# Kernel tuning notes

Hardware: AMD Instinct MI355X
Metric: run time of the kernel (lower is better)

## Reference

```python
import jax, jax.numpy as jnp
import numpy as np

NUM_CITIES = 88
NUM_YEARS = 6
STDDEVE = 0.01
STDDEVG = 0.1
STDDEVW = 0.1
N_ROWS = 200000


def setup_inputs() -> dict:
    key = jax.random.key(0)
    k = jax.random.split(key, 6)
    G = jax.random.normal(k[0], (N_ROWS, NUM_CITIES), dtype=jnp.float32)
    out = jax.random.normal(k[1], (N_ROWS, NUM_YEARS), dtype=jnp.float32)
    U = jax.random.normal(k[2], (N_ROWS, NUM_YEARS), dtype=jnp.float32)
    V = jax.random.normal(k[3], (N_ROWS, NUM_YEARS), dtype=jnp.float32)
    D = jax.random.normal(k[4], (N_ROWS, NUM_CITIES), dtype=jnp.float32)
    w = jax.random.normal(k[5], (N_ROWS, NUM_CITIES), dtype=jnp.float32)
    return {"G": G, "out": out, "U": U, "V": V, "D": D, "w": w}


def reference(G, out, U, V, D, w):
    # sum over first num_years-1 columns of ||U[:,i]-out[:,i]||_2^2 == Frobenius sq norm
    diff = U[:, : NUM_YEARS - 1] - out[:, : NUM_YEARS - 1]
    loss = jnp.sum(diff * diff)
    # sum_i log(||G[:,i]||_1), all 88 column L1 norms in one fused reduction
    lgg = jnp.sum(jnp.log(jnp.sum(jnp.abs(G), axis=0)))
    loss = loss + (STDDEVE ** 2) * lgg
    # ||G - w*D||_F^2 * stddevg^2 / stddeve^2
    r = G - w * D
    loss = loss + jnp.sum(r * r) * (STDDEVG ** 2 / STDDEVE ** 2)
    # ||w^2||_1 * stddeve^2 / stddevw^2
    loss = loss + jnp.sum(w * w) * (STDDEVE ** 2 / STDDEVW ** 2)
    # penalty: sum over negative entries of G, scaled by 100
    loss = loss + jnp.sum(jnp.where(G < 0, G, 0.0) * 100.0)
    return loss
```

## Files before the change

kernel.cpp:

```cpp
#include <hip/hip_runtime.h>
#include <math.h>

#define NUM_CITIES 88
#define NUM_YEARS 6
#define N_ROWS 200000

#define COL4 (NUM_CITIES / 4)
#define TOT4 (N_ROWS * COL4)
#define DIFF2 (N_ROWS * NUM_YEARS / 2)

#define NBLK 1936
#define NTHREADS (NBLK * 256)
#define NPART 92

#define TAIL_CUT (TOT4 - 8 * NTHREADS)

#define WS2_OFF (NBLK * NPART)

__global__ __launch_bounds__(256) void loss_main(
    const float* __restrict__ G,
    const float* __restrict__ outm,
    const float* __restrict__ U,
    const float* __restrict__ D,
    const float* __restrict__ w,
    float* __restrict__ ws)
{
    __shared__ float scol[NUM_CITIES];
    __shared__ float ssum[4];

    const int tid = threadIdx.x;
    const int gtid = blockIdx.x * blockDim.x + tid;
    const int c0 = (gtid % COL4) * 4;

    const float4* __restrict__ G4 = (const float4*)G;
    const float4* __restrict__ D4 = (const float4*)D;
    const float4* __restrict__ W4 = (const float4*)w;

    float4 g0 = G4[gtid + 0 * NTHREADS], g1 = G4[gtid + 1 * NTHREADS];
    float4 g2 = G4[gtid + 2 * NTHREADS], g3 = G4[gtid + 3 * NTHREADS];
    float4 g4 = G4[gtid + 4 * NTHREADS], g5 = G4[gtid + 5 * NTHREADS];
    float4 g6 = G4[gtid + 6 * NTHREADS], g7 = G4[gtid + 7 * NTHREADS];
    float4 d0 = D4[gtid + 0 * NTHREADS], d1 = D4[gtid + 1 * NTHREADS];
    float4 d2 = D4[gtid + 2 * NTHREADS], d3 = D4[gtid + 3 * NTHREADS];
    float4 d4 = D4[gtid + 4 * NTHREADS], d5 = D4[gtid + 5 * NTHREADS];
    float4 d6 = D4[gtid + 6 * NTHREADS], d7 = D4[gtid + 7 * NTHREADS];
    float4 v0 = W4[gtid + 0 * NTHREADS], v1 = W4[gtid + 1 * NTHREADS];
    float4 v2 = W4[gtid + 2 * NTHREADS], v3 = W4[gtid + 3 * NTHREADS];
    float4 v4 = W4[gtid + 4 * NTHREADS], v5 = W4[gtid + 5 * NTHREADS];
    float4 v6 = W4[gtid + 6 * NTHREADS], v7 = W4[gtid + 7 * NTHREADS];

    float ca0 = 0.f, ca1 = 0.f, ca2 = 0.f, ca3 = 0.f;
    float s_r2 = 0.f, s_w2 = 0.f, s_neg = 0.f;

#define ACC(g, d, v)                                                          \
    {                                                                         \
        ca0 += fabsf(g.x); ca1 += fabsf(g.y);                                 \
        ca2 += fabsf(g.z); ca3 += fabsf(g.w);                                 \
        float r0 = g.x - v.x * d.x, r1 = g.y - v.y * d.y;                     \
        float r2 = g.z - v.z * d.z, r3 = g.w - v.w * d.w;                     \
        s_r2 += r0 * r0 + r1 * r1 + r2 * r2 + r3 * r3;                        \
        s_w2 += v.x * v.x + v.y * v.y + v.z * v.z + v.w * v.w;                \
        s_neg += fminf(g.x, 0.f) + fminf(g.y, 0.f)                            \
               + fminf(g.z, 0.f) + fminf(g.w, 0.f);                           \
    }

    ACC(g0, d0, v0) ACC(g1, d1, v1) ACC(g2, d2, v2) ACC(g3, d3, v3)
    ACC(g4, d4, v4) ACC(g5, d5, v5) ACC(g6, d6, v6) ACC(g7, d7, v7)

    if (gtid < TAIL_CUT) {
        float4 g = G4[gtid + 8 * NTHREADS];
        float4 d = D4[gtid + 8 * NTHREADS];
        float4 v = W4[gtid + 8 * NTHREADS];
        ACC(g, d, v)
    }
#undef ACC

    const float2* __restrict__ U2 = (const float2*)U;
    const float2* __restrict__ O2 = (const float2*)outm;
    float s_diff = 0.f;
    {
        float2 u = U2[gtid], o = O2[gtid];
        float dx = u.x - o.x, dy = u.y - o.y;
        s_diff += dx * dx + ((gtid % 3 != 2) ? dy * dy : 0.f);
        const int i2 = gtid + NTHREADS;
        if (i2 < DIFF2) {
            float2 u2 = U2[i2], o2 = O2[i2];
            float ex = u2.x - o2.x, ey = u2.y - o2.y;
            s_diff += ex * ex + ((i2 % 3 != 2) ? ey * ey : 0.f);
        }
    }

    if (tid < NUM_CITIES) scol[tid] = 0.f;
    if (tid < 4) ssum[tid] = 0.f;
    __syncthreads();

    atomicAdd(&scol[c0 + 0], ca0);
    atomicAdd(&scol[c0 + 1], ca1);
    atomicAdd(&scol[c0 + 2], ca2);
    atomicAdd(&scol[c0 + 3], ca3);

    for (int off = 32; off > 0; off >>= 1) {
        s_diff += __shfl_down(s_diff, off);
        s_r2   += __shfl_down(s_r2, off);
        s_w2   += __shfl_down(s_w2, off);
        s_neg  += __shfl_down(s_neg, off);
    }
    if ((tid & 63) == 0) {
        atomicAdd(&ssum[0], s_diff);
        atomicAdd(&ssum[1], s_r2);
        atomicAdd(&ssum[2], s_w2);
        atomicAdd(&ssum[3], s_neg);
    }
    __syncthreads();

    float* dst = ws + (size_t)blockIdx.x * NPART;
    if (tid < NUM_CITIES) dst[tid] = scol[tid];
    else if (tid < NPART)  dst[tid] = ssum[tid - NUM_CITIES];
}

__global__ __launch_bounds__(256) void loss_reduce(float* __restrict__ ws)
{
    const int k = blockIdx.x;
    const int t = threadIdx.x;
    float acc = 0.f;
    for (int b = t; b < NBLK; b += 256)
        acc += ws[(size_t)b * NPART + k];
    for (int off = 32; off > 0; off >>= 1) acc += __shfl_down(acc, off);
    __shared__ float s[4];
    if ((t & 63) == 0) s[t >> 6] = acc;
    __syncthreads();
    if (t == 0) ws[WS2_OFF + k] = s[0] + s[1] + s[2] + s[3];
}

__global__ __launch_bounds__(128) void loss_finalize(
    const float* __restrict__ ws, float* __restrict__ out)
{
    __shared__ float sh[2];
    const int t = threadIdx.x;
    const float* ws2 = ws + WS2_OFF;

    float v = 0.f;
    if (t < NUM_CITIES)      v = 1e-4f * logf(ws2[t]);
    else if (t == 88)        v = ws2[88];
    else if (t == 89)        v = 100.f * ws2[89];
    else if (t == 90)        v = 0.01f * ws2[90];
    else if (t == 91)        v = 100.f * ws2[91];

    for (int off = 32; off > 0; off >>= 1) v += __shfl_down(v, off);
    if (t == 0)  sh[0] = v;
    if (t == 64) sh[1] = v;
    __syncthreads();
    if (t == 0) out[0] = sh[0] + sh[1];
}

extern "C" void kernel_launch(void* const* d_in, const int* in_sizes, int n_in,
                              void* d_out, int out_size, void* d_ws, size_t ws_size,
                              hipStream_t stream) {
    const float* G    = (const float*)d_in[0];
    const float* outm = (const float*)d_in[1];
    const float* U    = (const float*)d_in[2];
    const float* D    = (const float*)d_in[4];
    const float* w    = (const float*)d_in[5];
    float* out = (float*)d_out;
    float* ws  = (float*)d_ws;

    loss_main<<<NBLK, 256, 0, stream>>>(G, outm, U, D, w, ws);
    loss_reduce<<<NPART, 256, 0, stream>>>(ws);
    loss_finalize<<<1, 128, 0, stream>>>(ws, out);
}
```

Before: 224.8 us.

## Split G/D/w and U-out reductions into separate block groups with fewer items per thread

Restructures the main kernel so that most blocks each handle 4 float4 rows of G/D/w per thread, and a separate set of blocks handles the U-out difference with float4 loads in a grid-stride loop. The aim is to raise the number of threads and outstanding loads, and to stop the large G/D/w loads from being serialized with the small difference loads in the same thread. In exchange there are many more blocks, each doing a full shared-memory column reduction and writing 92 partials, so the second reduction pass reads about 2.4 times as many partials.

```diff
diff --git a/kernel.cpp b/kernel.cpp
--- a/kernel.cpp
+++ b/kernel.cpp
@@ -5,17 +5,17 @@
 #define NUM_YEARS 6
 #define N_ROWS 200000
 
-#define COL4 (NUM_CITIES / 4)
-#define TOT4 (N_ROWS * COL4)
-#define DIFF2 (N_ROWS * NUM_YEARS / 2)
+#define TOT4 (N_ROWS * 22)
+#define NT   (TOT4 / 4)
+#define GBLK 4297
 
-#define NBLK 1936
-#define NTHREADS (NBLK * 256)
+#define NQ4  (N_ROWS * NUM_YEARS / 4)
+#define DTHREADS 75008
+#define DBLK 293
+
+#define NBLK_TOT (GBLK + DBLK)
 #define NPART 92
-
-#define TAIL_CUT (TOT4 - 8 * NTHREADS)
-
-#define WS2_OFF (NBLK * NPART)
+#define WS2_OFF (NBLK_TOT * NPART)
 
 __global__ __launch_bounds__(256) void loss_main(
     const float* __restrict__ G,
@@ -29,75 +29,66 @@
     __shared__ float ssum[4];
 
     const int tid = threadIdx.x;
-    const int gtid = blockIdx.x * blockDim.x + tid;
-    const int c0 = (gtid % COL4) * 4;
-
-    const float4* __restrict__ G4 = (const float4*)G;
-    const float4* __restrict__ D4 = (const float4*)D;
-    const float4* __restrict__ W4 = (const float4*)w;
-
-    float4 g0 = G4[gtid + 0 * NTHREADS], g1 = G4[gtid + 1 * NTHREADS];
-    float4 g2 = G4[gtid + 2 * NTHREADS], g3 = G4[gtid + 3 * NTHREADS];
-    float4 g4 = G4[gtid + 4 * NTHREADS], g5 = G4[gtid + 5 * NTHREADS];
-    float4 g6 = G4[gtid + 6 * NTHREADS], g7 = G4[gtid + 7 * NTHREADS];
-    float4 d0 = D4[gtid + 0 * NTHREADS], d1 = D4[gtid + 1 * NTHREADS];
-    float4 d2 = D4[gtid + 2 * NTHREADS], d3 = D4[gtid + 3 * NTHREADS];
-    float4 d4 = D4[gtid + 4 * NTHREADS], d5 = D4[gtid + 5 * NTHREADS];
-    float4 d6 = D4[gtid + 6 * NTHREADS], d7 = D4[gtid + 7 * NTHREADS];
-    float4 v0 = W4[gtid + 0 * NTHREADS], v1 = W4[gtid + 1 * NTHREADS];
-    float4 v2 = W4[gtid + 2 * NTHREADS], v3 = W4[gtid + 3 * NTHREADS];
-    float4 v4 = W4[gtid + 4 * NTHREADS], v5 = W4[gtid + 5 * NTHREADS];
-    float4 v6 = W4[gtid + 6 * NTHREADS], v7 = W4[gtid + 7 * NTHREADS];
-
-    float ca0 = 0.f, ca1 = 0.f, ca2 = 0.f, ca3 = 0.f;
-    float s_r2 = 0.f, s_w2 = 0.f, s_neg = 0.f;
-
-#define ACC(g, d, v)                                                          \
-    {                                                                         \
-        ca0 += fabsf(g.x); ca1 += fabsf(g.y);                                 \
-        ca2 += fabsf(g.z); ca3 += fabsf(g.w);                                 \
-        float r0 = g.x - v.x * d.x, r1 = g.y - v.y * d.y;                     \
-        float r2 = g.z - v.z * d.z, r3 = g.w - v.w * d.w;                     \
-        s_r2 += r0 * r0 + r1 * r1 + r2 * r2 + r3 * r3;                        \
-        s_w2 += v.x * v.x + v.y * v.y + v.z * v.z + v.w * v.w;                \
-        s_neg += fminf(g.x, 0.f) + fminf(g.y, 0.f)                            \
-               + fminf(g.z, 0.f) + fminf(g.w, 0.f);                           \
-    }
-
-    ACC(g0, d0, v0) ACC(g1, d1, v1) ACC(g2, d2, v2) ACC(g3, d3, v3)
-    ACC(g4, d4, v4) ACC(g5, d5, v5) ACC(g6, d6, v6) ACC(g7, d7, v7)
-
-    if (gtid < TAIL_CUT) {
-        float4 g = G4[gtid + 8 * NTHREADS];
-        float4 d = D4[gtid + 8 * NTHREADS];
-        float4 v = W4[gtid + 8 * NTHREADS];
-        ACC(g, d, v)
-    }
-#undef ACC
-
-    const float2* __restrict__ U2 = (const float2*)U;
-    const float2* __restrict__ O2 = (const float2*)outm;
-    float s_diff = 0.f;
-    {
-        float2 u = U2[gtid], o = O2[gtid];
-        float dx = u.x - o.x, dy = u.y - o.y;
-        s_diff += dx * dx + ((gtid % 3 != 2) ? dy * dy : 0.f);
-        const int i2 = gtid + NTHREADS;
-        if (i2 < DIFF2) {
-            float2 u2 = U2[i2], o2 = O2[i2];
-            float ex = u2.x - o2.x, ey = u2.y - o2.y;
-            s_diff += ex * ex + ((i2 % 3 != 2) ? ey * ey : 0.f);
-        }
-    }
+    const int bid = blockIdx.x;
 
     if (tid < NUM_CITIES) scol[tid] = 0.f;
     if (tid < 4) ssum[tid] = 0.f;
     __syncthreads();
 
-    atomicAdd(&scol[c0 + 0], ca0);
-    atomicAdd(&scol[c0 + 1], ca1);
-    atomicAdd(&scol[c0 + 2], ca2);
-    atomicAdd(&scol[c0 + 3], ca3);
+    float s_diff = 0.f, s_r2 = 0.f, s_w2 = 0.f, s_neg = 0.f;
+
+    if (bid < GBLK) {
+        const int i = bid * 256 + tid;
+        const int c0 = (i % 22) * 4;
+        float ca0 = 0.f, ca1 = 0.f, ca2 = 0.f, ca3 = 0.f;
+
+        if (i < NT) {
+            const float4* __restrict__ G4 = (const float4*)G;
+            const float4* __restrict__ D4 = (const float4*)D;
+            const float4* __restrict__ W4 = (const float4*)w;
+
+            float4 g0 = G4[i + 0 * NT], g1 = G4[i + 1 * NT];
+            float4 g2 = G4[i + 2 * NT], g3 = G4[i + 3 * NT];
+            float4 d0 = D4[i + 0 * NT], d1 = D4[i + 1 * NT];
+            float4 d2 = D4[i + 2 * NT], d3 = D4[i + 3 * NT];
+            float4 v0 = W4[i + 0 * NT], v1 = W4[i + 1 * NT];
+            float4 v2 = W4[i + 2 * NT], v3 = W4[i + 3 * NT];
+
+#define ACC(g, d, v)                                                          \
+            {                                                                 \
+                ca0 += fabsf(g.x); ca1 += fabsf(g.y);                         \
+                ca2 += fabsf(g.z); ca3 += fabsf(g.w);                         \
+                float r0 = g.x - v.x * d.x, r1 = g.y - v.y * d.y;             \
+                float r2 = g.z - v.z * d.z, r3 = g.w - v.w * d.w;             \
+                s_r2 += r0 * r0 + r1 * r1 + r2 * r2 + r3 * r3;                \
+                s_w2 += v.x * v.x + v.y * v.y + v.z * v.z + v.w * v.w;        \
+                s_neg += fminf(g.x, 0.f) + fminf(g.y, 0.f)                    \
+                       + fminf(g.z, 0.f) + fminf(g.w, 0.f);                   \
+            }
+            ACC(g0, d0, v0) ACC(g1, d1, v1) ACC(g2, d2, v2) ACC(g3, d3, v3)
+#undef ACC
+        }
+
+        atomicAdd(&scol[c0 + 0], ca0);
+        atomicAdd(&scol[c0 + 1], ca1);
+        atomicAdd(&scol[c0 + 2], ca2);
+        atomicAdd(&scol[c0 + 3], ca3);
+    } else {
+        const float4* __restrict__ U4 = (const float4*)U;
+        const float4* __restrict__ O4 = (const float4*)outm;
+        const int dtid = (bid - GBLK) * 256 + tid;
+        #pragma unroll 4
+        for (int q = dtid; q < NQ4; q += DTHREADS) {
+            float4 u = U4[q];
+            float4 o = O4[q];
+            float ex = u.x - o.x, ey = u.y - o.y;
+            float ez = u.z - o.z, ew = u.w - o.w;
+            int ph = q % 3;
+            s_diff += ex * ex + ez * ez;
+            s_diff += (ph == 1) ? 0.f : ey * ey;
+            s_diff += (ph == 2) ? 0.f : ew * ew;
+        }
+    }
 
     for (int off = 32; off > 0; off >>= 1) {
         s_diff += __shfl_down(s_diff, off);
@@ -113,8 +104,8 @@
     }
     __syncthreads();
 
-    float* dst = ws + (size_t)blockIdx.x * NPART;
-    if (tid < NUM_CITIES) dst[tid] = scol[tid];
+    float* dst = ws + (size_t)bid * NPART;
+    if (tid < NUM_CITIES)  dst[tid] = scol[tid];
     else if (tid < NPART)  dst[tid] = ssum[tid - NUM_CITIES];
 }
 
@@ -123,7 +114,7 @@
     const int k = blockIdx.x;
     const int t = threadIdx.x;
     float acc = 0.f;
-    for (int b = t; b < NBLK; b += 256)
+    for (int b = t; b < NBLK_TOT; b += 256)
         acc += ws[(size_t)b * NPART + k];
     for (int off = 32; off > 0; off >>= 1) acc += __shfl_down(acc, off);
     __shared__ float s[4];
@@ -164,7 +155,7 @@
     float* out = (float*)d_out;
     float* ws  = (float*)d_ws;
 
-    loss_main<<<NBLK, 256, 0, stream>>>(G, outm, U, D, w, ws);
+    loss_main<<<NBLK_TOT, 256, 0, stream>>>(G, outm, U, D, w, ws);
     loss_reduce<<<NPART, 256, 0, stream>>>(ws);
     loss_finalize<<<1, 128, 0, stream>>>(ws, out);
 }
```

Result: no change. 228.4 us (+1.6%).
